# Kernel tuning notes

Measured on AMD Instinct MI355X. Metric: run time of the kernel, lower is better.

The kernel has to match this reference:

```python
import jax, jax.numpy as jnp
import numpy as np

D_MODEL = 1024
D_STATE = 128
D_CONV = 4
EXPAND = 2
HEADDIM = 64
D_INNER = EXPAND * D_MODEL          # 2048
NHEADS = D_INNER // HEADDIM          # 32
CONV_CH = D_INNER + 2 * D_STATE      # conv acts on x, B, C (ngroups=1)
D_IN_PROJ = 2 * D_INNER + 2 * D_STATE + NHEADS
CHUNK = 128


def setup_inputs() -> dict:
    key = jax.random.key(0)
    ks = jax.random.split(key, 8)
    B, L = 4, 2048
    return {
        'x': jax.random.normal(ks[0], (B, L, D_MODEL), jnp.float32),
        'ln_w': jnp.ones((D_MODEL,), jnp.float32),
        'ln_b': jnp.zeros((D_MODEL,), jnp.float32),
        'in_proj_w': jax.random.normal(ks[1], (D_IN_PROJ, D_MODEL), jnp.float32) * 0.02,
        'conv_w': jax.random.normal(ks[2], (CONV_CH, D_CONV), jnp.float32) * 0.2,
        'conv_b': jnp.zeros((CONV_CH,), jnp.float32),
        'dt_bias': jax.random.normal(ks[3], (NHEADS,), jnp.float32) * 0.5,
        'A_log': jax.random.uniform(ks[4], (NHEADS,), jnp.float32, 0.0, 1.5),
        'D': jax.random.normal(ks[5], (NHEADS,), jnp.float32) * 0.1 + 1.0,
        'norm_w': jnp.ones((D_INNER,), jnp.float32),
        'out_proj_w': jax.random.normal(ks[6], (D_MODEL, D_INNER), jnp.float32) * 0.02,
    }


def segsum(a):
    # a: (..., T) -> (..., T, T) with out[i, j] = sum_{j < k <= i} a[k], -inf above diag
    T = a.shape[-1]
    a_rep = jnp.broadcast_to(a[..., :, None], a.shape + (T,))
    a_masked = jnp.where(jnp.tril(jnp.ones((T, T), bool), -1), a_rep, 0.0)
    seg = jnp.cumsum(a_masked, axis=-2)
    return jnp.where(jnp.tril(jnp.ones((T, T), bool), 0), seg, -jnp.inf)


def _ssd(X, a, Bm, Cm):
    # Chunked SSD (Mamba2). X: (b,l,h,p) pre-multiplied by dt; a: (b,l,h)=dt*A; Bm,Cm: (b,l,n)
    b, l, h, p = X.shape
    c = l // CHUNK
    Xc = X.reshape(b, c, CHUNK, h, p)
    Bc = Bm.reshape(b, c, CHUNK, -1)
    Cc = Cm.reshape(b, c, CHUNK, -1)
    ac = a.reshape(b, c, CHUNK, h).transpose(0, 3, 1, 2)   # (b,h,c,q)
    a_cs = jnp.cumsum(ac, axis=-1)                          # (b,h,c,q)
    Lm = jnp.exp(segsum(ac))                                # (b,h,c,q,q)
    # intra-chunk (diagonal) part
    Y_diag = jnp.einsum('bcln,bcsn,bhcls,bcshp->bclhp', Cc, Bc, Lm, Xc)
    # chunk final states
    decay_states = jnp.exp(a_cs[..., -1:] - a_cs)           # (b,h,c,q)
    states = jnp.einsum('bcln,bhcl,bclhp->bchpn', Bc, decay_states, Xc)
    states = jnp.concatenate([jnp.zeros_like(states[:, :1]), states], axis=1)  # (b,c+1,h,p,n)
    a_chunk = jnp.pad(a_cs[..., -1], ((0, 0), (0, 0), (1, 0)))  # (b,h,c+1)
    decay_chunk = jnp.exp(segsum(a_chunk))                  # (b,h,c+1,c+1)
    prev_states = jnp.einsum('bhzc,bchpn->bzhpn', decay_chunk, states)[:, :-1]  # (b,c,h,p,n)
    # inter-chunk (off-diagonal) part
    Y_off = jnp.einsum('bcln,bchpn,bhcl->bclhp', Cc, prev_states, jnp.exp(a_cs))
    return (Y_diag + Y_off).reshape(b, l, h, p)


def reference(x, ln_w, ln_b, in_proj_w, conv_w, conv_b, dt_bias, A_log, D, norm_w, out_proj_w):
    B, L, _ = x.shape
    # pre-LayerNorm
    mu = x.mean(-1, keepdims=True)
    var = ((x - mu) ** 2).mean(-1, keepdims=True)
    h = (x - mu) / jnp.sqrt(var + 1e-5) * ln_w + ln_b
    # Mamba2 in_proj -> [z, xBC, dt]
    zxbcdt = h @ in_proj_w.T
    z = zxbcdt[..., :D_INNER]
    xBC = zxbcdt[..., D_INNER:D_INNER + CONV_CH]
    dt = jax.nn.softplus(zxbcdt[..., -NHEADS:] + dt_bias)  # (B,L,H)
    # causal depthwise conv1d + SiLU
    xp = jnp.pad(xBC, ((0, 0), (D_CONV - 1, 0), (0, 0)))
    conv = sum(xp[:, k:k + L, :] * conv_w[:, k] for k in range(D_CONV)) + conv_b
    xBC = jax.nn.silu(conv)
    xs = xBC[..., :D_INNER].reshape(B, L, NHEADS, HEADDIM)
    Bm = xBC[..., D_INNER:D_INNER + D_STATE]
    Cm = xBC[..., D_INNER + D_STATE:]
    A = -jnp.exp(A_log)                                    # (H,)
    Y = _ssd(xs * dt[..., None], dt * A, Bm, Cm)
    Y = Y + D[None, None, :, None] * xs                    # D skip connection
    y = Y.reshape(B, L, D_INNER)
    # gated RMSNorm (norm_before_gate=False)
    y = y * jax.nn.silu(z)
    y = y * jax.lax.rsqrt(jnp.mean(y * y, -1, keepdims=True) + 1e-5) * norm_w
    out = y @ out_proj_w.T
    # dropout in eval mode = identity; residual
    return out + x
```

## Files before the change

### kernel.cpp

```cpp
#include <hip/hip_runtime.h>
#include <math.h>

#define BATCH   4
#define LSEQ    2048
#define DMODEL  1024
#define DSTATE  128
#define HEADDIM 64
#define DINNER  2048
#define NHEADS  32
#define CONVCH  2304
#define DINPROJ 4384
#define NPAD    4608
#define CHUNKL  128
#define NCHUNK  16
#define ROWS    (BATCH*LSEQ)

#define B_Z     ((size_t)0)
#define B_XBC   (B_Z   + (size_t)ROWS*DINNER*2)
#define B_DT    (B_XBC + (size_t)ROWS*CONVCH*2)
#define B_XS    (B_DT  + (size_t)ROWS*NHEADS*4)
#define B_BC    (B_XS  + (size_t)ROWS*DINNER*2)
#define B_Y     (B_BC  + (size_t)ROWS*256*2)
#define B_ASUM  (B_Y   + (size_t)ROWS*DINNER*2)
#define B_END   (B_ASUM + (size_t)BATCH*NCHUNK*NHEADS*4)

typedef __attribute__((ext_vector_type(8))) short bf16x8;
typedef __attribute__((ext_vector_type(4))) float f32x4;

__device__ __forceinline__ float b2f(ushort u) {
  union { uint32_t i; float f; } v; v.i = ((uint32_t)u) << 16; return v.f;
}
__device__ __forceinline__ ushort f2b(float f) {
  union { float f; uint32_t i; } v; v.f = f;
  uint32_t r = (v.i + 0x7FFFu + ((v.i >> 16) & 1u)) >> 16;
  return (ushort)r;
}

__device__ __forceinline__ void async_ld16(const void* g, void* l) {
  __builtin_amdgcn_global_load_lds(
      (const __attribute__((address_space(1))) unsigned int*)g,
      (__attribute__((address_space(3))) unsigned int*)l, 16, 0, 0);
}

#define VMG(n) asm volatile("s_waitcnt vmcnt(" #n ")" ::: "memory")


template<int K>
__device__ __forceinline__ void stage_half(const ushort* __restrict__ M,
    int row0, int k0, int tid, ushort* dst)
{
  #pragma unroll
  for (int it = 0; it < 2; it++) {
    int s = it*512 + tid;
    int rl = s >> 3;
    int g = (s & 7) ^ (rl & 7);
    async_ld16(M + (size_t)(row0 + rl)*K + k0 + g*8, dst + (size_t)s*8);
  }
}

template<int QM, int QN, bool RDA>
__device__ __forceinline__ void qphase(const ushort* __restrict__ bA,
    const ushort* __restrict__ bB, int wq, int wn, int rl, int q,
    bf16x8 (&af)[2][4], bf16x8 (&bfr)[2][2], f32x4 (&acc)[2][2][4][2])
{
  __builtin_amdgcn_s_barrier();
  __builtin_amdgcn_sched_barrier(0);
  if (RDA) {
    #pragma unroll
    for (int kh = 0; kh < 2; kh++)
      #pragma unroll
      for (int ii = 0; ii < 4; ii++) {
        int row = QM*128 + wq*64 + ii*16 + rl;
        af[kh][ii] = *(const bf16x8*)&bA[(size_t)(row*8 + ((kh*4 + q) ^ (row & 7)))*8];
      }
  }
  #pragma unroll
  for (int kh = 0; kh < 2; kh++)
    #pragma unroll
    for (int jj = 0; jj < 2; jj++) {
      int row = QN*128 + wn*32 + jj*16 + rl;
      bfr[kh][jj] = *(const bf16x8*)&bB[(size_t)(row*8 + ((kh*4 + q) ^ (row & 7)))*8];
    }
  __builtin_amdgcn_s_setprio(1);
  #pragma unroll
  for (int kh = 0; kh < 2; kh++)
    #pragma unroll
    for (int ii = 0; ii < 4; ii++)
      #pragma unroll
      for (int jj = 0; jj < 2; jj++)
        acc[QM][QN][ii][jj] = __builtin_amdgcn_mfma_f32_16x16x32_bf16(
            af[kh][ii], bfr[kh][jj], acc[QM][QN][ii][jj], 0, 0, 0);
  __builtin_amdgcn_s_setprio(0);
  __builtin_amdgcn_sched_barrier(0);
  __builtin_amdgcn_s_barrier();
}

template<int K>
__device__ __forceinline__ void stage_tile(const ushort* __restrict__ A,
    const ushort* __restrict__ W, int m0, int n0, int tid, int t,
    ushort* lA, ushort* lB)
{
  const int k0 = t * 64;
  #pragma unroll
  for (int it = 0; it < 4; it++) {
    int s = it*512 + tid;
    int row = s >> 3;
    int g = (s & 7) ^ (row & 7);
    async_ld16(A + (size_t)(m0 + row)*K + k0 + g*8, lA + (size_t)s*8);
  }
  #pragma unroll
  for (int it = 0; it < 2; it++) {
    int s = it*512 + tid;
    int row = s >> 3;
    int g = (s & 7) ^ (row & 7);
    async_ld16(W + (size_t)(n0 + row)*K + k0 + g*8, lB + (size_t)s*8);
  }
}

__device__ __forceinline__ void compute_tile(const ushort* lA, const ushort* lB,
    int wr, int wc, int rl, int q, f32x4 acc[4][4])
{
  #pragma unroll
  for (int kh = 0; kh < 2; kh++) {
    bf16x8 af[4], bfr[4];
    #pragma unroll
    for (int i = 0; i < 4; i++) {
      int row = wr*64 + i*16 + rl;
      af[i] = *(const bf16x8*)&lA[(size_t)(row*8 + ((kh*4 + q) ^ (row & 7)))*8];
    }
    #pragma unroll
    for (int j = 0; j < 4; j++) {
      int row = wc*64 + j*16 + rl;
      bfr[j] = *(const bf16x8*)&lB[(size_t)(row*8 + ((kh*4 + q) ^ (row & 7)))*8];
    }
    #pragma unroll
    for (int i = 0; i < 4; i++)
      #pragma unroll
      for (int j = 0; j < 4; j++)
        acc[i][j] = __builtin_amdgcn_mfma_f32_16x16x32_bf16(af[i], bfr[j], acc[i][j], 0, 0, 0);
  }
}

__global__ __launch_bounds__(256) void convert_win_kernel(const float* __restrict__ W,
                                                          ushort* __restrict__ Wb)
{
  size_t i = (size_t)blockIdx.x*256 + threadIdx.x;
  Wb[i] = (i < (size_t)DINPROJ*DMODEL) ? f2b(W[i]) : (ushort)0;
}

__global__ __launch_bounds__(256) void convert_wout_kernel(const float* __restrict__ W,
                                                           ushort* __restrict__ Wb)
{
  size_t i = (size_t)blockIdx.x*256 + threadIdx.x;
  Wb[i] = f2b(W[i]);
}

__global__ __launch_bounds__(256) void ln_kernel(const float* __restrict__ x,
    const float* __restrict__ w, const float* __restrict__ bias, ushort* __restrict__ h)
{
  const int row = blockIdx.x;
  const int t = threadIdx.x;
  const float* xr = x + (size_t)row * DMODEL;
  float v[4];
  float s = 0.f;
  #pragma unroll
  for (int i = 0; i < 4; i++) { v[i] = xr[t + i*256]; s += v[i]; }
  __shared__ float red[4];
  #pragma unroll
  for (int o = 32; o > 0; o >>= 1) s += __shfl_down(s, o, 64);
  if ((t & 63) == 0) red[t >> 6] = s;
  __syncthreads();
  float mean = (red[0]+red[1]+red[2]+red[3]) * (1.f/DMODEL);
  float vs = 0.f;
  #pragma unroll
  for (int i = 0; i < 4; i++) { float d = v[i]-mean; vs += d*d; }
  #pragma unroll
  for (int o = 32; o > 0; o >>= 1) vs += __shfl_down(vs, o, 64);
  __syncthreads();
  if ((t & 63) == 0) red[t >> 6] = vs;
  __syncthreads();
  float rstd = rsqrtf((red[0]+red[1]+red[2]+red[3]) * (1.f/DMODEL) + 1e-5f);
  ushort* hr = h + (size_t)row * DMODEL;
  #pragma unroll
  for (int i = 0; i < 4; i++) {
    int c = t + i*256;
    hr[c] = f2b((v[i]-mean)*rstd*w[c] + bias[c]);
  }
}

__global__ __launch_bounds__(512, 1) void gemm_inproj_8ph(const ushort* __restrict__ A,
    const ushort* __restrict__ W, ushort* __restrict__ z, ushort* __restrict__ xbc,
    float* __restrict__ dtr, const float* __restrict__ dtb)
{
  __shared__ ushort smem[65536];
  const int tid = threadIdx.x;
  const int lane = tid & 63;
  const int w = tid >> 6;
  const int wq = w >> 2;
  const int wn = w & 3;
  const int rl = lane & 15;
  const int q  = lane >> 4;

  const int orig = blockIdx.x;
  const int xcd  = orig & 7;
  const int jj_  = orig >> 3;
  const int m0 = (xcd*4 + jj_/18) * 256;
  const int n0 = (jj_ % 18) * 256;

  f32x4 acc[2][2][4][2];
  #pragma unroll
  for (int a = 0; a < 2; a++)
    #pragma unroll
    for (int b = 0; b < 2; b++)
      #pragma unroll
      for (int c = 0; c < 4; c++)
        #pragma unroll
        for (int d = 0; d < 2; d++) acc[a][b][c][d] = (f32x4)(0.f);

  bf16x8 af[2][4], bfr[2][2];
  constexpr int NT = DMODEL / 64;

  {
    ushort* A0 = smem;            ushort* B0 = smem + 16384;
    ushort* A1 = smem + 32768;    ushort* B1 = A1 + 16384;
    stage_half<DMODEL>(A, m0+0,   0,  tid, A0);
    stage_half<DMODEL>(W, n0+0,   0,  tid, B0);
    stage_half<DMODEL>(W, n0+128, 0,  tid, B0 + 8192);
    stage_half<DMODEL>(A, m0+128, 0,  tid, A0 + 8192);
    stage_half<DMODEL>(A, m0+0,   64, tid, A1);
    stage_half<DMODEL>(W, n0+0,   64, tid, B1);
  }

  for (int t = 0; t < NT-2; t++) {
    const int d = t & 1;
    const ushort* bA = smem + d*32768;
    const ushort* bB = bA + 16384;
    ushort* nA = smem + (d^1)*32768;
    ushort* nB = nA + 16384;
    ushort* sA = smem + d*32768;
    ushort* sB = sA + 16384;
    stage_half<DMODEL>(W, n0+128, (t+1)*64, tid, nB + 8192);
    VMG(10);
    qphase<0,0,true >(bA, bB, wq, wn, rl, q, af, bfr, acc);
    stage_half<DMODEL>(A, m0+128, (t+1)*64, tid, nA + 8192);
    VMG(10);
    qphase<0,1,false>(bA, bB, wq, wn, rl, q, af, bfr, acc);
    stage_half<DMODEL>(A, m0+0, (t+2)*64, tid, sA);
    VMG(10);
    qphase<1,0,true >(bA, bB, wq, wn, rl, q, af, bfr, acc);
    stage_half<DMODEL>(W, n0+0, (t+2)*64, tid, sB);
    qphase<1,1,false>(bA, bB, wq, wn, rl, q, af, bfr, acc);
  }
  {
    const int t = NT-2;
    const int d = t & 1;
    const ushort* bA = smem + d*32768;
    const ushort* bB = bA + 16384;
    ushort* nA = smem + (d^1)*32768;
    ushort* nB = nA + 16384;
    stage_half<DMODEL>(W, n0+128, (t+1)*64, tid, nB + 8192);
    VMG(10);
    qphase<0,0,true >(bA, bB, wq, wn, rl, q, af, bfr, acc);
    stage_half<DMODEL>(A, m0+128, (t+1)*64, tid, nA + 8192);
    VMG(10);
    qphase<0,1,false>(bA, bB, wq, wn, rl, q, af, bfr, acc);
    VMG(8);
    qphase<1,0,true >(bA, bB, wq, wn, rl, q, af, bfr, acc);
    qphase<1,1,false>(bA, bB, wq, wn, rl, q, af, bfr, acc);
  }
  {
    const int t = NT-1;
    const int d = t & 1;
    const ushort* bA = smem + d*32768;
    const ushort* bB = bA + 16384;
    VMG(4);
    qphase<0,0,true >(bA, bB, wq, wn, rl, q, af, bfr, acc);
    VMG(2);
    qphase<0,1,false>(bA, bB, wq, wn, rl, q, af, bfr, acc);
    VMG(0);
    qphase<1,0,true >(bA, bB, wq, wn, rl, q, af, bfr, acc);
    qphase<1,1,false>(bA, bB, wq, wn, rl, q, af, bfr, acc);
  }

  const int colL = lane & 15;
  const int rowQ = (lane >> 4) * 4;
  if (n0 < DINNER + CONVCH) {
    #pragma unroll
    for (int qm = 0; qm < 2; qm++)
      #pragma unroll
      for (int qn = 0; qn < 2; qn++)
        #pragma unroll
        for (int ii = 0; ii < 4; ii++)
          #pragma unroll
          for (int jj = 0; jj < 2; jj++) {
            int col = qn*128 + wn*32 + jj*16 + colL;
            int g = col >> 3;
            #pragma unroll
            for (int r = 0; r < 4; r++) {
              int row = qm*128 + wq*64 + ii*16 + rowQ + r;
              int p = (g & 24) | ((g ^ row) & 7);
              smem[row*256 + p*8 + (col & 7)] = f2b(acc[qm][qn][ii][jj][r]);
            }
          }
    __syncthreads();
    ushort* outp; int coff, ncols;
    if (n0 < DINNER) { outp = z;   coff = n0;          ncols = DINNER; }
    else             { outp = xbc; coff = n0 - DINNER; ncols = CONVCH; }
    #pragma unroll
    for (int it = 0; it < 16; it++) {
      int idx = tid + it*512;
      int row = idx >> 5, g = idx & 31;
      int p = (g & 24) | ((g ^ row) & 7);
      *(uint4*)(outp + (size_t)(m0 + row)*ncols + coff + g*8) =
          *(const uint4*)&smem[row*256 + p*8];
    }
  } else {
    if (wn == 0) {
      #pragma unroll
      for (int qm = 0; qm < 2; qm++)
        #pragma unroll
        for (int ii = 0; ii < 4; ii++)
          #pragma unroll
          for (int jj = 0; jj < 2; jj++) {
            int lc = jj*16 + colL;
            float bb = dtb[lc];
            #pragma unroll
            for (int r = 0; r < 4; r++) {
              float v = acc[qm][0][ii][jj][r] + bb;
              v = (v > 20.f) ? v : log1pf(expf(v));
              dtr[(size_t)(m0 + qm*128 + wq*64 + ii*16 + rowQ + r)*NHEADS + lc] = v;
            }
          }
    }
  }
}

__global__ __launch_bounds__(512, 1) void gemm_outproj_big(const ushort* __restrict__ A,
    const ushort* __restrict__ W, const float* __restrict__ x, float* __restrict__ out)
{
  __shared__ ushort smem[49152];
  ushort* lA0 = smem;
  ushort* lB0 = smem + 32768;
  float* fbuf = (float*)smem;
  const int tid = threadIdx.x;
  const int lane = tid & 63;
  const int w = tid >> 6;
  const int wr = w >> 1;
  const int wc = w & 1;
  const int rl = lane & 15;
  const int q  = lane >> 4;

  const int orig = blockIdx.x;
  const int xcd  = orig & 7;
  const int jj   = orig >> 3;
  const int m0 = (xcd*4 + (jj >> 3)) * 256;
  const int n0 = (jj & 7) * 128;

  f32x4 acc[4][4];
  #pragma unroll
  for (int i = 0; i < 4; i++)
    #pragma unroll
    for (int j = 0; j < 4; j++) acc[i][j] = (f32x4)(0.f);

  constexpr int NT = DINNER / 64;
  stage_tile<DINNER>(A, W, m0, n0, tid, 0, lA0, lB0);
  for (int t = 0; t < NT; t++) {
    const ushort* cA = lA0 + (size_t)(t & 1) * 16384;
    const ushort* cB = lB0 + (size_t)(t & 1) * 8192;
    if (t + 1 < NT) {
      stage_tile<DINNER>(A, W, m0, n0, tid, t + 1,
                         lA0 + (size_t)((t+1) & 1) * 16384,
                         lB0 + (size_t)((t+1) & 1) * 8192);
      asm volatile("s_waitcnt vmcnt(6)" ::: "memory");
    } else {
      asm volatile("s_waitcnt vmcnt(0)" ::: "memory");
    }
    __builtin_amdgcn_s_barrier();
    __builtin_amdgcn_sched_barrier(0);
    __builtin_amdgcn_s_setprio(1);
    compute_tile(cA, cB, wr, wc, rl, q, acc);
    __builtin_amdgcn_s_setprio(0);
    __builtin_amdgcn_sched_barrier(0);
    __builtin_amdgcn_s_barrier();
  }

  const int colL = lane & 15;
  const int rowQ = (lane >> 4) * 4;
  #pragma unroll
  for (int h = 0; h < 2; h++) {
    __syncthreads();
    if ((wr >> 1) == h) {
      #pragma unroll
      for (int i = 0; i < 4; i++)
        #pragma unroll
        for (int j = 0; j < 4; j++) {
          int col = wc*64 + j*16 + colL;
          int g = col >> 2;
          #pragma unroll
          for (int r = 0; r < 4; r++) {
            int row = (wr & 1)*64 + i*16 + rowQ + r;
            fbuf[row*128 + ((g ^ (row & 7)) << 2) + (col & 3)] = acc[i][j][r];
          }
        }
    }
    __syncthreads();
    #pragma unroll
    for (int it = 0; it < 8; it++) {
      int idx = tid + it*512;
      int row = idx >> 5, c4 = idx & 31;
      int gm = m0 + h*128 + row;
      float4 xv = *(const float4*)(x + (size_t)gm*DMODEL + n0 + c4*4);
      float4 vv = *(const float4*)&fbuf[row*128 + ((c4 ^ (row & 7)) << 2)];
      vv.x += xv.x; vv.y += xv.y; vv.z += xv.z; vv.w += xv.w;
      *(float4*)(out + (size_t)gm*DMODEL + n0 + c4*4) = vv;
    }
  }
}

__global__ __launch_bounds__(256) void conv_tiled(const ushort* __restrict__ xbc,
    const float* __restrict__ cw, const float* __restrict__ cb,
    ushort* __restrict__ xs, ushort* __restrict__ bcb)
{
  __shared__ ushort tile[35*256];
  const int tid = threadIdx.x;
  const int ch0 = blockIdx.x * 256;
  const int row0 = blockIdx.y * 32;
  const int l0 = row0 & (LSEQ-1);
  for (int idx = tid; idx < 35*32; idx += 256) {
    int r = idx >> 5, c16 = idx & 31;
    uint4 v = make_uint4(0,0,0,0);
    if (l0 + r - 3 >= 0)
      v = *(const uint4*)(xbc + (size_t)(row0 + r - 3)*CONVCH + ch0 + c16*8);
    *(uint4*)&tile[r*256 + c16*8] = v;
  }
  __syncthreads();
  const int ch = ch0 + tid;
  const float w0 = cw[ch*4+0], w1 = cw[ch*4+1], w2 = cw[ch*4+2], w3 = cw[ch*4+3];
  const float bias = cb[ch];
  const bool isX = (ch0 < DINNER);
  #pragma unroll 4
  for (int r = 0; r < 32; r++) {
    float acc = bias;
    acc = fmaf(b2f(tile[(r+0)*256 + tid]), w0, acc);
    acc = fmaf(b2f(tile[(r+1)*256 + tid]), w1, acc);
    acc = fmaf(b2f(tile[(r+2)*256 + tid]), w2, acc);
    acc = fmaf(b2f(tile[(r+3)*256 + tid]), w3, acc);
    float v = acc / (1.f + expf(-acc));
    if (isX) xs[(size_t)(row0 + r)*DINNER + ch] = f2b(v);
    else     bcb[(size_t)(row0 + r)*256 + (ch - DINNER)] = f2b(v);
  }
}

__global__ __launch_bounds__(256) void states_mfma(
    const ushort* __restrict__ xs, const ushort* __restrict__ bcb, const float* __restrict__ dt,
    const float* __restrict__ A_log, ushort* __restrict__ S, float* __restrict__ asum)
{
  constexpr int LDP = 136;
  __shared__ ushort lBT[128*LDP];
  __shared__ ushort lXT[64*LDP];
  __shared__ float dts[CHUNKL], acs[CHUNKL];
  __shared__ float wtot;
  const int hh = blockIdx.x, c = blockIdx.y, b = blockIdx.z;
  const int tid = threadIdx.x;
  const int lane = tid & 63;
  const int w = tid >> 6;
  const int rbase = b*LSEQ + c*CHUNKL;
  const size_t sbase = (size_t)((b*NCHUNK + c)*NHEADS + hh) * 8192;

  float pre = 0.f;
  if (tid < 128) {
    float myv = dt[(size_t)(rbase + tid)*NHEADS + hh];
    dts[tid] = myv;
    pre = myv;
    #pragma unroll
    for (int o = 1; o < 64; o <<= 1) {
      float u = __shfl_up(pre, o, 64);
      if ((tid & 63) >= o) pre += u;
    }
    if (tid == 63) wtot = pre;
  }
  #pragma unroll
  for (int it = 0; it < 8; it++) {
    int chunk = tid + it*256;
    int l = chunk >> 4, n8 = chunk & 15;
    ushort tmp[8];
    *(uint4*)tmp = *(const uint4*)(bcb + (size_t)(rbase + l)*256 + n8*8);
    #pragma unroll
    for (int u = 0; u < 8; u++) lBT[(n8*8+u)*LDP + l] = tmp[u];
  }
  __syncthreads();
  float alast_loc = 0.f;
  if (tid < 128) {
    float Aval = -expf(A_log[hh]);
    float a = (pre + ((tid >= 64) ? wtot : 0.f)) * Aval;
    acs[tid] = a;
    if (tid == 127) { asum[(b*NCHUNK + c)*NHEADS + hh] = a; }
  }
  __syncthreads();
  alast_loc = acs[CHUNKL-1];
  #pragma unroll
  for (int it = 0; it < 4; it++) {
    int chunk = tid + it*256;
    int l = chunk >> 3, p8 = (chunk & 7)*8;
    ushort tmp[8];
    *(uint4*)tmp = *(const uint4*)(xs + (size_t)(rbase + l)*DINNER + hh*HEADDIM + p8);
    float wl = dts[l] * expf(alast_loc - acs[l]);
    #pragma unroll
    for (int u = 0; u < 8; u++) lXT[(p8+u)*LDP + l] = f2b(b2f(tmp[u]) * wl);
  }
  __syncthreads();

  const int rl = lane & 15;
  const int kq = (lane >> 4) * 8;
  const int nb = w * 32;
  f32x4 acc[4][2];
  #pragma unroll
  for (int i = 0; i < 4; i++) { acc[i][0] = (f32x4)(0.f); acc[i][1] = (f32x4)(0.f); }
  #pragma unroll
  for (int k0 = 0; k0 < 128; k0 += 32) {
    bf16x8 af[4], bfr[2];
    #pragma unroll
    for (int i = 0; i < 4; i++) af[i]  = *(const bf16x8*)&lXT[(i*16 + rl)*LDP + k0 + kq];
    #pragma unroll
    for (int j = 0; j < 2; j++) bfr[j] = *(const bf16x8*)&lBT[(nb + j*16 + rl)*LDP + k0 + kq];
    #pragma unroll
    for (int i = 0; i < 4; i++)
      #pragma unroll
      for (int j = 0; j < 2; j++)
        acc[i][j] = __builtin_amdgcn_mfma_f32_16x16x32_bf16(af[i], bfr[j], acc[i][j], 0, 0, 0);
  }
  __syncthreads();
  const int colL = lane & 15;
  const int rowQ = (lane >> 4) * 4;
  #pragma unroll
  for (int i = 0; i < 4; i++)
    #pragma unroll
    for (int j = 0; j < 2; j++)
      #pragma unroll
      for (int r = 0; r < 4; r++)
        lXT[(i*16 + rowQ + r)*LDP + nb + j*16 + colL] = f2b(acc[i][j][r]);
  __syncthreads();
  #pragma unroll
  for (int it = 0; it < 4; it++) {
    int idx = tid + it*256;
    int row = idx >> 4, c8 = idx & 15;
    *(uint4*)(S + sbase + row*128 + c8*8) = *(const uint4*)&lXT[row*LDP + c8*8];
  }
}

__global__ __launch_bounds__(256) void scan_kernel(ushort* __restrict__ S, const float* __restrict__ asum)
{
  const int hh = blockIdx.x, sl = blockIdx.y, b = blockIdx.z;
  const int base0 = sl*2048 + threadIdx.x;
  float carry[8];
  #pragma unroll
  for (int i = 0; i < 8; i++) carry[i] = 0.f;
  for (int c = 0; c < NCHUNK; c++) {
    ushort* Sp = S + (size_t)((b*NCHUNK + c)*NHEADS + hh) * 8192;
    float dec = expf(asum[(b*NCHUNK + c)*NHEADS + hh]);
    #pragma unroll
    for (int i = 0; i < 8; i++) {
      int idx = base0 + i*256;
      float sv = b2f(Sp[idx]);
      Sp[idx] = f2b(carry[i]);
      carry[i] = fmaf(dec, carry[i], sv);
    }
  }
}

__global__ __launch_bounds__(256) void yssd_mfma(
    const ushort* __restrict__ xs, const ushort* __restrict__ bcb, const float* __restrict__ dt,
    const float* __restrict__ A_log, const float* __restrict__ Dvec,
    const ushort* __restrict__ S, ushort* __restrict__ y)
{
  constexpr int LDP = 136;
  __shared__ ushort lM [128*LDP];
  __shared__ ushort lXT[64*LDP];
  __shared__ float dts[CHUNKL], acs[CHUNKL];
  __shared__ float wtot;
  const int hh = blockIdx.x, c = blockIdx.y, b = blockIdx.z;
  const int tid = threadIdx.x;
  const int lane = tid & 63;
  const int w = tid >> 6;
  const int rbase = b*LSEQ + c*CHUNKL;
  const size_t sbase = (size_t)((b*NCHUNK + c)*NHEADS + hh) * 8192;
  const ushort* Bg = bcb + (size_t)rbase*256;
  const ushort* Cg = Bg + 128;

  #pragma unroll
  for (int it = 0; it < 4; it++) {
    int chunk = tid + it*256;
    int s = chunk >> 3, p0 = (chunk & 7)*8;
    ushort tmp[8];
    *(uint4*)tmp = *(const uint4*)(xs + (size_t)(rbase + s)*DINNER + hh*HEADDIM + p0);
    #pragma unroll
    for (int u = 0; u < 8; u++) lXT[(p0+u)*LDP + s] = tmp[u];
  }
  float pre = 0.f;
  if (tid < 128) {
    float myv = dt[(size_t)(rbase + tid)*NHEADS + hh];
    dts[tid] = myv;
    pre = myv;
    #pragma unroll
    for (int o = 1; o < 64; o <<= 1) {
      float u = __shfl_up(pre, o, 64);
      if ((tid & 63) >= o) pre += u;
    }
    if (tid == 63) wtot = pre;
  }
  __syncthreads();
  if (tid < 128) {
    float Aval = -expf(A_log[hh]);
    acs[tid] = (pre + ((tid >= 64) ? wtot : 0.f)) * Aval;
  }

  const int rl = lane & 15;
  const int kq = (lane >> 4) * 8;
  const int colL = lane & 15;
  const int rowQ = (lane >> 4) * 4;

  const int wm = (w & 1) * 64;
  const int wn = (w >> 1) * 64;
  f32x4 G[4][4];
  #pragma unroll
  for (int i = 0; i < 4; i++)
    #pragma unroll
    for (int j = 0; j < 4; j++) G[i][j] = (f32x4)(0.f);
  #pragma unroll
  for (int k0 = 0; k0 < 128; k0 += 32) {
    bf16x8 af[4], bfr[4];
    #pragma unroll
    for (int i = 0; i < 4; i++) af[i]  = *(const bf16x8*)(Cg + (size_t)(wm + i*16 + rl)*256 + k0 + kq);
    #pragma unroll
    for (int j = 0; j < 4; j++) bfr[j] = *(const bf16x8*)(Bg + (size_t)(wn + j*16 + rl)*256 + k0 + kq);
    #pragma unroll
    for (int i = 0; i < 4; i++)
      #pragma unroll
      for (int j = 0; j < 4; j++)
        G[i][j] = __builtin_amdgcn_mfma_f32_16x16x32_bf16(af[i], bfr[j], G[i][j], 0, 0, 0);
  }
  __syncthreads();

  #pragma unroll
  for (int j = 0; j < 4; j++) {
    int sIdx = wn + j*16 + colL;
    float as = acs[sIdx];
    float ds = dts[sIdx];
    #pragma unroll
    for (int i = 0; i < 4; i++) {
      #pragma unroll
      for (int r = 0; r < 4; r++) {
        int lIdx = wm + i*16 + rowQ + r;
        float m = (lIdx >= sIdx) ? G[i][j][r] * expf(acs[lIdx] - as) * ds : 0.f;
        lM[lIdx*LDP + sIdx] = f2b(m);
      }
    }
  }

  const int om = w * 32;
  f32x4 Y[2][4];
  #pragma unroll
  for (int i = 0; i < 2; i++)
    #pragma unroll
    for (int j = 0; j < 4; j++) Y[i][j] = (f32x4)(0.f);
  #pragma unroll
  for (int k0 = 0; k0 < 128; k0 += 32) {
    bf16x8 a2[2], b2[4];
    #pragma unroll
    for (int i = 0; i < 2; i++) a2[i] = *(const bf16x8*)(Cg + (size_t)(om + i*16 + rl)*256 + k0 + kq);
    #pragma unroll
    for (int j = 0; j < 4; j++) b2[j] = *(const bf16x8*)(S + sbase + (size_t)(j*16 + rl)*128 + k0 + kq);
    #pragma unroll
    for (int i = 0; i < 2; i++)
      #pragma unroll
      for (int j = 0; j < 4; j++)
        Y[i][j] = __builtin_amdgcn_mfma_f32_16x16x32_bf16(a2[i], b2[j], Y[i][j], 0, 0, 0);
  }
  #pragma unroll
  for (int i = 0; i < 2; i++)
    #pragma unroll
    for (int r = 0; r < 4; r++) {
      float e = expf(acs[om + i*16 + rowQ + r]);
      #pragma unroll
      for (int j = 0; j < 4; j++) Y[i][j][r] *= e;
    }
  __syncthreads();

  #pragma unroll
  for (int k0 = 0; k0 < 128; k0 += 32) {
    bf16x8 a3[2], b3[4];
    #pragma unroll
    for (int i = 0; i < 2; i++) a3[i] = *(const bf16x8*)&lM[(om + i*16 + rl)*LDP + k0 + kq];
    #pragma unroll
    for (int j = 0; j < 4; j++) b3[j] = *(const bf16x8*)&lXT[(j*16 + rl)*LDP + k0 + kq];
    #pragma unroll
    for (int i = 0; i < 2; i++)
      #pragma unroll
      for (int j = 0; j < 4; j++)
        Y[i][j] = __builtin_amdgcn_mfma_f32_16x16x32_bf16(a3[i], b3[j], Y[i][j], 0, 0, 0);
  }

  const float Dh = Dvec[hh];
  #pragma unroll
  for (int i = 0; i < 2; i++) {
    #pragma unroll
    for (int r = 0; r < 4; r++) {
      int lIdx = om + i*16 + rowQ + r;
      ushort* yrow = y + (size_t)(rbase + lIdx)*DINNER + hh*HEADDIM;
      #pragma unroll
      for (int j = 0; j < 4; j++) {
        int p = j*16 + colL;
        float val = Y[i][j][r] + Dh * b2f(lXT[p*LDP + lIdx]);
        yrow[p] = f2b(val);
      }
    }
  }
}

__global__ __launch_bounds__(256) void rmsnorm_kernel(ushort* __restrict__ y,
    const ushort* __restrict__ z, const float* __restrict__ nw)
{
  const int row = blockIdx.x;
  const int t = threadIdx.x;
  ushort* yr = y + (size_t)row*DINNER;
  const ushort* zr = z + (size_t)row*DINNER;
  float v[8];
  float ss = 0.f;
  #pragma unroll
  for (int i = 0; i < 8; i++) {
    int c = t + i*256;
    float zz = b2f(zr[c]);
    float g = b2f(yr[c]) * (zz / (1.f + expf(-zz)));
    v[i] = g;
    ss += g*g;
  }
  #pragma unroll
  for (int o = 32; o > 0; o >>= 1) ss += __shfl_down(ss, o, 64);
  __shared__ float red[4];
  if ((t & 63) == 0) red[t >> 6] = ss;
  __syncthreads();
  float scale = rsqrtf((red[0]+red[1]+red[2]+red[3]) * (1.f/DINNER) + 1e-5f);
  #pragma unroll
  for (int i = 0; i < 8; i++) {
    int c = t + i*256;
    yr[c] = f2b(v[i]*scale*nw[c]);
  }
}

extern "C" void kernel_launch(void* const* d_in, const int* in_sizes, int n_in,
                              void* d_out, int out_size, void* d_ws, size_t ws_size,
                              hipStream_t stream)
{
  const float* x    = (const float*)d_in[0];
  const float* lnw  = (const float*)d_in[1];
  const float* lnb  = (const float*)d_in[2];
  const float* win  = (const float*)d_in[3];
  const float* cw   = (const float*)d_in[4];
  const float* cb   = (const float*)d_in[5];
  const float* dtb  = (const float*)d_in[6];
  const float* alog = (const float*)d_in[7];
  const float* dvec = (const float*)d_in[8];
  const float* nw   = (const float*)d_in[9];
  const float* wout = (const float*)d_in[10];
  float* out = (float*)d_out;
  char* ws = (char*)d_ws;
  (void)in_sizes; (void)n_in; (void)out_size;

  if (ws_size < B_END) return;

  ushort* zb   = (ushort*)(ws + B_Z);
  ushort* xbcb = (ushort*)(ws + B_XBC);
  float*  dtr  = (float*) (ws + B_DT);
  ushort* xsb  = (ushort*)(ws + B_XS);
  ushort* bcb  = (ushort*)(ws + B_BC);
  ushort* yb   = (ushort*)(ws + B_Y);
  float*  asum = (float*) (ws + B_ASUM);
  ushort* Sb   = xbcb;
  ushort* hb   = yb;
  ushort* winB = (ushort*)(ws + B_Y + (size_t)ROWS*DMODEL*2);
  ushort* woutB= (ushort*)(ws + B_XBC + (size_t)BATCH*NCHUNK*NHEADS*HEADDIM*DSTATE*2);

  hipLaunchKernelGGL(convert_win_kernel, dim3((NPAD*DMODEL)/256), dim3(256), 0, stream, win, winB);
  hipLaunchKernelGGL(ln_kernel, dim3(ROWS), dim3(256), 0, stream, x, lnw, lnb, hb);
  hipLaunchKernelGGL(gemm_inproj_8ph, dim3(576), dim3(512), 0, stream, hb, winB, zb, xbcb, dtr, dtb);
  hipLaunchKernelGGL(conv_tiled, dim3(9, ROWS/32), dim3(256), 0, stream, xbcb, cw, cb, xsb, bcb);
  hipLaunchKernelGGL(convert_wout_kernel, dim3((DMODEL*DINNER)/256), dim3(256), 0, stream, wout, woutB);
  hipLaunchKernelGGL(states_mfma, dim3(NHEADS, NCHUNK, BATCH), dim3(256), 0, stream,
                     xsb, bcb, dtr, alog, Sb, asum);
  hipLaunchKernelGGL(scan_kernel, dim3(NHEADS, 4, BATCH), dim3(256), 0, stream, Sb, asum);
  hipLaunchKernelGGL(yssd_mfma, dim3(NHEADS, NCHUNK, BATCH), dim3(256), 0, stream,
                     xsb, bcb, dtr, alog, dvec, Sb, yb);
  hipLaunchKernelGGL(rmsnorm_kernel, dim3(ROWS), dim3(256), 0, stream, yb, zb, nw);
  hipLaunchKernelGGL(gemm_outproj_big, dim3(256), dim3(512), 0, stream, yb, woutB, x, out);
}
```

Measured before the change: 476.2 us.

## Restructure in_proj GEMM pipeline to overlap LDS reads with async global loads

Splits each quadrant phase into separate LDS fragment reads and an MFMA block, issuing the global-to-LDS stage loads between the reads and the barrier-guarded MFMA. The staging order is changed and the wait counts are reworked so that each whole k-tile is waited on once, at the end of an iteration, instead of waiting before every quadrant. The goal is to hide LDS read latency and cut the number of vmcnt stalls in the main GEMM loop. It relies on fairly subtle barrier and waitcnt ordering, so a mistake in the async-copy hazards could cause races.

Measured after the change: 468.7 us. Within noise of the previous version (-1.6%).

```diff
diff --git a/kernel.cpp b/kernel.cpp
--- a/kernel.cpp
+++ b/kernel.cpp
@@ -59,12 +59,10 @@
 }
 
 template<int QM, int QN, bool RDA>
-__device__ __forceinline__ void qphase(const ushort* __restrict__ bA,
+__device__ __forceinline__ void qreads(const ushort* __restrict__ bA,
     const ushort* __restrict__ bB, int wq, int wn, int rl, int q,
-    bf16x8 (&af)[2][4], bf16x8 (&bfr)[2][2], f32x4 (&acc)[2][2][4][2])
-{
-  __builtin_amdgcn_s_barrier();
-  __builtin_amdgcn_sched_barrier(0);
+    bf16x8 (&af)[2][4], bf16x8 (&bfr)[2][2])
+{
   if (RDA) {
     #pragma unroll
     for (int kh = 0; kh < 2; kh++)
@@ -81,6 +79,16 @@
       int row = QN*128 + wn*32 + jj*16 + rl;
       bfr[kh][jj] = *(const bf16x8*)&bB[(size_t)(row*8 + ((kh*4 + q) ^ (row & 7)))*8];
     }
+}
+
+template<int QM, int QN>
+__device__ __forceinline__ void qmma(bf16x8 (&af)[2][4], bf16x8 (&bfr)[2][2],
+    f32x4 (&acc)[2][2][4][2])
+{
+  __builtin_amdgcn_sched_barrier(0);
+  __builtin_amdgcn_s_barrier();
+  asm volatile("s_waitcnt lgkmcnt(0)" ::: "memory");
+  __builtin_amdgcn_sched_barrier(0);
   __builtin_amdgcn_s_setprio(1);
   #pragma unroll
   for (int kh = 0; kh < 2; kh++)
@@ -225,10 +233,13 @@
     ushort* A1 = smem + 32768;    ushort* B1 = A1 + 16384;
     stage_half<DMODEL>(A, m0+0,   0,  tid, A0);
     stage_half<DMODEL>(W, n0+0,   0,  tid, B0);
+    stage_half<DMODEL>(A, m0+128, 0,  tid, A0 + 8192);
     stage_half<DMODEL>(W, n0+128, 0,  tid, B0 + 8192);
-    stage_half<DMODEL>(A, m0+128, 0,  tid, A0 + 8192);
     stage_half<DMODEL>(A, m0+0,   64, tid, A1);
     stage_half<DMODEL>(W, n0+0,   64, tid, B1);
+    VMG(4);
+    __builtin_amdgcn_s_barrier();
+    __builtin_amdgcn_sched_barrier(0);
   }
 
   for (int t = 0; t < NT-2; t++) {
@@ -239,17 +250,19 @@
     ushort* nB = nA + 16384;
     ushort* sA = smem + d*32768;
     ushort* sB = sA + 16384;
+    qreads<0,0,true >(bA, bB, wq, wn, rl, q, af, bfr);
+    stage_half<DMODEL>(A, m0+128, (t+1)*64, tid, nA + 8192);
+    qmma<0,0>(af, bfr, acc);
+    qreads<0,1,false>(bA, bB, wq, wn, rl, q, af, bfr);
     stage_half<DMODEL>(W, n0+128, (t+1)*64, tid, nB + 8192);
-    VMG(10);
-    qphase<0,0,true >(bA, bB, wq, wn, rl, q, af, bfr, acc);
-    stage_half<DMODEL>(A, m0+128, (t+1)*64, tid, nA + 8192);
-    VMG(10);
-    qphase<0,1,false>(bA, bB, wq, wn, rl, q, af, bfr, acc);
+    qmma<0,1>(af, bfr, acc);
+    qreads<1,0,true >(bA, bB, wq, wn, rl, q, af, bfr);
     stage_half<DMODEL>(A, m0+0, (t+2)*64, tid, sA);
-    VMG(10);
-    qphase<1,0,true >(bA, bB, wq, wn, rl, q, af, bfr, acc);
+    qmma<1,0>(af, bfr, acc);
+    qreads<1,1,false>(bA, bB, wq, wn, rl, q, af, bfr);
     stage_half<DMODEL>(W, n0+0, (t+2)*64, tid, sB);
-    qphase<1,1,false>(bA, bB, wq, wn, rl, q, af, bfr, acc);
+    VMG(4);
+    qmma<1,1>(af, bfr, acc);
   }
   {
     const int t = NT-2;
@@ -258,28 +271,30 @@
     const ushort* bB = bA + 16384;
     ushort* nA = smem + (d^1)*32768;
     ushort* nB = nA + 16384;
+    qreads<0,0,true >(bA, bB, wq, wn, rl, q, af, bfr);
+    stage_half<DMODEL>(A, m0+128, (t+1)*64, tid, nA + 8192);
+    qmma<0,0>(af, bfr, acc);
+    qreads<0,1,false>(bA, bB, wq, wn, rl, q, af, bfr);
     stage_half<DMODEL>(W, n0+128, (t+1)*64, tid, nB + 8192);
-    VMG(10);
-    qphase<0,0,true >(bA, bB, wq, wn, rl, q, af, bfr, acc);
-    stage_half<DMODEL>(A, m0+128, (t+1)*64, tid, nA + 8192);
-    VMG(10);
-    qphase<0,1,false>(bA, bB, wq, wn, rl, q, af, bfr, acc);
-    VMG(8);
-    qphase<1,0,true >(bA, bB, wq, wn, rl, q, af, bfr, acc);
-    qphase<1,1,false>(bA, bB, wq, wn, rl, q, af, bfr, acc);
+    qmma<0,1>(af, bfr, acc);
+    qreads<1,0,true >(bA, bB, wq, wn, rl, q, af, bfr);
+    qmma<1,0>(af, bfr, acc);
+    qreads<1,1,false>(bA, bB, wq, wn, rl, q, af, bfr);
+    VMG(0);
+    qmma<1,1>(af, bfr, acc);
   }
   {
-    const int t = NT-1;
-    const int d = t & 1;
+    const int d = (NT-1) & 1;
     const ushort* bA = smem + d*32768;
     const ushort* bB = bA + 16384;
-    VMG(4);
-    qphase<0,0,true >(bA, bB, wq, wn, rl, q, af, bfr, acc);
-    VMG(2);
-    qphase<0,1,false>(bA, bB, wq, wn, rl, q, af, bfr, acc);
-    VMG(0);
-    qphase<1,0,true >(bA, bB, wq, wn, rl, q, af, bfr, acc);
-    qphase<1,1,false>(bA, bB, wq, wn, rl, q, af, bfr, acc);
+    qreads<0,0,true >(bA, bB, wq, wn, rl, q, af, bfr);
+    qmma<0,0>(af, bfr, acc);
+    qreads<0,1,false>(bA, bB, wq, wn, rl, q, af, bfr);
+    qmma<0,1>(af, bfr, acc);
+    qreads<1,0,true >(bA, bB, wq, wn, rl, q, af, bfr);
+    qmma<1,0>(af, bfr, acc);
+    qreads<1,1,false>(bA, bB, wq, wn, rl, q, af, bfr);
+    qmma<1,1>(af, bfr, acc);
   }
 
   const int colL = lane & 15;
```
